# Kernel tuning notes

Hardware: AMD Instinct MI355X
Metric: run time of the kernel (lower is better)

The kernel has to match this reference:

```python
import jax, jax.numpy as jnp
import numpy as np

EMBED_DIM = 512
NUM_HEADS = 8
HEAD_DIM = EMBED_DIM // NUM_HEADS
SCALE = HEAD_DIM ** -0.5
B, N = 4, 2048


def setup_inputs() -> dict:
    key = jax.random.key(0)
    ks = jax.random.split(key, 6)
    x = jax.random.normal(ks[0], (B, N, EMBED_DIM), dtype=jnp.float32)
    mask = jnp.ones((B, N, N), dtype=jnp.int32)
    # nn.Linear params: weight [out, in], bias [out]
    lim_qkv = 1.0 / np.sqrt(EMBED_DIM)
    qkv_w = jax.random.uniform(ks[1], (3 * EMBED_DIM, EMBED_DIM), jnp.float32, -lim_qkv, lim_qkv)
    qkv_b = jax.random.uniform(ks[2], (3 * EMBED_DIM,), jnp.float32, -lim_qkv, lim_qkv)
    proj_w = jax.random.uniform(ks[3], (EMBED_DIM, EMBED_DIM), jnp.float32, -lim_qkv, lim_qkv)
    proj_b = jax.random.uniform(ks[4], (EMBED_DIM,), jnp.float32, -lim_qkv, lim_qkv)
    return {"x": x, "qkv_w": qkv_w, "qkv_b": qkv_b, "proj_w": proj_w, "proj_b": proj_b, "mask": mask}


def reference(x, qkv_w, qkv_b, proj_w, proj_b, mask):
    Bb, Nn, C = x.shape
    qkv = (jnp.einsum('bnc,oc->bno', x, qkv_w) + qkv_b).reshape(Bb, Nn, 3, NUM_HEADS, HEAD_DIM)
    qkv = jnp.transpose(qkv, (2, 0, 3, 1, 4))
    q, k, v = qkv[0], qkv[1], qkv[2]
    # full score matrix [B,H,N,N] (faithful to the unfused original)
    attn = jnp.einsum('bhnd,bhmd->bhnm', q, k) * SCALE
    attn = jnp.where(mask[:, None, :, :] == 0, -jnp.inf, attn)
    attn = jax.nn.softmax(attn, axis=-1)
    out = jnp.einsum('bhnm,bhmd->bhnd', attn, v)
    out = jnp.transpose(out, (0, 2, 1, 3)).reshape(Bb, Nn, C)
    out = jnp.einsum('bnc,oc->bno', out, proj_w) + proj_b
    return out
```

## Files before the change

kernel.cpp:

```cpp
#include <hip/hip_runtime.h>
#include <hip/hip_bf16.h>
#include <stdint.h>

#define NB 4
#define NH 8
#define SEQ 2048
#define HD 64
#define CDIM 512

using bf16 = __hip_bfloat16;
typedef __attribute__((ext_vector_type(8))) short short8;
typedef __attribute__((ext_vector_type(4))) short short4_t;
typedef __attribute__((ext_vector_type(4))) float f32x4;

#define NEG_BIG (-3.0e38f)
#define SOFT_C 0.18033688011112042f

__device__ __forceinline__ short bf16_bits(float x) {
  return __builtin_bit_cast(short, __float2bfloat16(x));
}

#define X4 1048576
#define Q4 196608
#define P4 65536
__global__ __launch_bounds__(256) void prep_cvt(const float* __restrict__ x,
                                                const float* __restrict__ wq,
                                                const float* __restrict__ wp,
                                                short* __restrict__ xb,
                                                short* __restrict__ wqb,
                                                short* __restrict__ wpb) {
  int idx = blockIdx.x * 256 + threadIdx.x;
  int stride = gridDim.x * 256;
  for (int i = idx; i < X4 + Q4 + P4; i += stride) {
    const float* src; short* dst; int off;
    if (i < X4)            { src = x;  dst = xb;  off = i; }
    else if (i < X4 + Q4)  { src = wq; dst = wqb; off = i - X4; }
    else                   { src = wp; dst = wpb; off = i - X4 - Q4; }
    f32x4 v = *(const f32x4*)(src + (size_t)off * 4);
    short4_t o;
    o[0] = bf16_bits(v[0]); o[1] = bf16_bits(v[1]);
    o[2] = bf16_bits(v[2]); o[3] = bf16_bits(v[3]);
    *(short4_t*)(dst + (size_t)off * 4) = o;
  }
}

__global__ __launch_bounds__(256) void qkv_union(const short* __restrict__ Xb,
                                                 const short* __restrict__ Wb,
                                                 const float* __restrict__ bias,
                                                 const int* __restrict__ mask,
                                                 unsigned long long* __restrict__ bits,
                                                 bf16* __restrict__ q,
                                                 bf16* __restrict__ k,
                                                 bf16* __restrict__ vt) {
  __shared__ short Alds[128][40];
  __shared__ short Blds[128][40];
  const int tid = threadIdx.x;
  const int lane = tid & 63;
  const int w = tid >> 6;

  if (blockIdx.x < 512) {
    int wave_g = blockIdx.x * 4 + w;
#pragma unroll 1
    for (int i = 0; i < 32; i++) {
      size_t c = (size_t)i * 2048 + wave_g;
      size_t base = c * 256;
      int v0 = mask[base + 0 * 64 + lane];
      int v1 = mask[base + 1 * 64 + lane];
      int v2 = mask[base + 2 * 64 + lane];
      int v3 = mask[base + 3 * 64 + lane];
      unsigned long long w0 = __ballot(v0 != 0);
      unsigned long long w1 = __ballot(v1 != 0);
      unsigned long long w2 = __ballot(v2 != 0);
      unsigned long long w3 = __ballot(v3 != 0);
      if (lane == 0) {
        bits[c * 4 + 0] = w0; bits[c * 4 + 1] = w1;
        bits[c * 4 + 2] = w2; bits[c * 4 + 3] = w3;
      }
    }
    return;
  }

  const int g = blockIdx.x - 512;
  const int wm = w >> 1, wn = w & 1;
  const int row0 = (g & 63) * 128;
  const int col0 = (g >> 6) * 128;

  f32x4 acc[4][4] = {};
  const int lr = tid >> 2;
  const int lc = (tid & 3) * 8;
  const int cl = lane & 15;
  const int koff = (lane >> 4) * 8;

  for (int kk = 0; kk < 512; kk += 32) {
    *(short8*)&Alds[lr][lc]      = *(const short8*)&Xb[(size_t)(row0 + lr) * 512 + kk + lc];
    *(short8*)&Alds[lr + 64][lc] = *(const short8*)&Xb[(size_t)(row0 + lr + 64) * 512 + kk + lc];
    *(short8*)&Blds[lr][lc]      = *(const short8*)&Wb[(size_t)(col0 + lr) * 512 + kk + lc];
    *(short8*)&Blds[lr + 64][lc] = *(const short8*)&Wb[(size_t)(col0 + lr + 64) * 512 + kk + lc];
    __syncthreads();
    short8 a[4], b[4];
#pragma unroll
    for (int i = 0; i < 4; i++) a[i] = *(const short8*)&Alds[wm * 64 + i * 16 + cl][koff];
#pragma unroll
    for (int j = 0; j < 4; j++) b[j] = *(const short8*)&Blds[wn * 64 + j * 16 + cl][koff];
#pragma unroll
    for (int i = 0; i < 4; i++)
#pragma unroll
      for (int j = 0; j < 4; j++)
        acc[i][j] = __builtin_amdgcn_mfma_f32_16x16x32_bf16(a[i], b[j], acc[i][j], 0, 0, 0);
    __syncthreads();
  }

#pragma unroll
  for (int i = 0; i < 4; i++) {
#pragma unroll
    for (int j = 0; j < 4; j++) {
      int col = col0 + wn * 64 + j * 16 + cl;
      float bv = bias[col];
      int which = col >> 9;
      int c = col & 511;
      int h = c >> 6, d = c & 63;
#pragma unroll
      for (int r = 0; r < 4; r++) {
        int row = row0 + wm * 64 + i * 16 + (lane >> 4) * 4 + r;
        int bb = row >> 11, n = row & 2047;
        float val = acc[i][j][r] + bv;
        size_t bh = (size_t)bb * NH + h;
        if (which == 0)      q[(bh * SEQ + n) * HD + d] = __float2bfloat16(val * SOFT_C);
        else if (which == 1) k[(bh * SEQ + n) * HD + d] = __float2bfloat16(val);
        else                 vt[(bh * HD + d) * SEQ + n] = __float2bfloat16(val);
      }
    }
  }
}

__global__ __launch_bounds__(256) void flash_attn(const bf16* __restrict__ qg,
                                                  const bf16* __restrict__ kg,
                                                  const bf16* __restrict__ vg,
                                                  const unsigned long long* __restrict__ mbits,
                                                  bf16* __restrict__ attn_out) {
  __shared__ short Klds[64][72];
  __shared__ short Vlds[64][72];
  __shared__ short Plds[4][16][72];
  __shared__ unsigned long long Mlds[64];

  const int tid = threadIdx.x;
  const int lane = tid & 63;
  const int w = tid >> 6;
  const int qt = blockIdx.x;
  const int h = blockIdx.y;
  const int b = blockIdx.z;

  const size_t bh = (size_t)b * NH + h;
  const bf16* qp = qg + bh * SEQ * HD;
  const bf16* kp = kg + bh * SEQ * HD;
  const bf16* vp = vg + bh * HD * SEQ;

  const int cl = lane & 15;
  const int quad = lane >> 4;
  const int koff = quad * 8;
  const int qrow_w = qt * 64 + w * 16;

  short8 aq0 = *(const short8*)&qp[(size_t)(qrow_w + cl) * HD + koff];
  short8 aq1 = *(const short8*)&qp[(size_t)(qrow_w + cl) * HD + 32 + koff];

  f32x4 o[4] = {};
  float l_l = 0.f;

  const int sr = tid >> 3;
  const int sc = (tid & 7) * 8;

  for (int kt = 0; kt < 32; kt++) {
    const int kb = kt * 64;
    *(short8*)&Klds[sr][sc]      = *(const short8*)&kp[(size_t)(kb + sr) * HD + sc];
    *(short8*)&Klds[sr + 32][sc] = *(const short8*)&kp[(size_t)(kb + sr + 32) * HD + sc];
    *(short8*)&Vlds[sr][sc]      = *(const short8*)&vp[(size_t)sr * SEQ + kb + sc];
    *(short8*)&Vlds[sr + 32][sc] = *(const short8*)&vp[(size_t)(sr + 32) * SEQ + kb + sc];
    if (tid < 64) Mlds[tid] = mbits[((size_t)b * SEQ + qt * 64 + tid) * (SEQ / 64) + kt];
    __syncthreads();

    f32x4 s[4];
#pragma unroll
    for (int nb = 0; nb < 4; nb++) {
      short8 k0 = *(const short8*)&Klds[nb * 16 + cl][koff];
      short8 k1 = *(const short8*)&Klds[nb * 16 + cl][32 + koff];
      f32x4 z = {0.f, 0.f, 0.f, 0.f};
      z = __builtin_amdgcn_mfma_f32_16x16x32_bf16(k0, aq0, z, 0, 0, 0);
      s[nb] = __builtin_amdgcn_mfma_f32_16x16x32_bf16(k1, aq1, z, 0, 0, 0);
    }

    unsigned long long wd = Mlds[w * 16 + cl];
    if (wd != ~0ULL) {
#pragma unroll
      for (int nb = 0; nb < 4; nb++)
#pragma unroll
        for (int r = 0; r < 4; r++)
          if (!((wd >> (nb * 16 + quad * 4 + r)) & 1ULL)) s[nb][r] = NEG_BIG;
    }

    float ps = 0.f;
#pragma unroll
    for (int nb = 0; nb < 4; nb++)
#pragma unroll
      for (int r = 0; r < 4; r++) {
        float p = exp2f(s[nb][r]);
        s[nb][r] = p;
        ps += p;
      }
    ps += __shfl_xor(ps, 16);
    ps += __shfl_xor(ps, 32);
    l_l += ps;

#pragma unroll
    for (int nb = 0; nb < 4; nb++) {
      short4_t pk;
      pk[0] = bf16_bits(s[nb][0]); pk[1] = bf16_bits(s[nb][1]);
      pk[2] = bf16_bits(s[nb][2]); pk[3] = bf16_bits(s[nb][3]);
      *(short4_t*)&Plds[w][cl][nb * 16 + quad * 4] = pk;
    }

#pragma unroll
    for (int ks = 0; ks < 2; ks++) {
      short8 pa = *(const short8*)&Plds[w][cl][ks * 32 + koff];
#pragma unroll
      for (int db = 0; db < 4; db++) {
        short8 vb = *(const short8*)&Vlds[db * 16 + cl][ks * 32 + koff];
        o[db] = __builtin_amdgcn_mfma_f32_16x16x32_bf16(pa, vb, o[db], 0, 0, 0);
      }
    }
    __syncthreads();
  }

  float inv = 1.0f / l_l;
#pragma unroll
  for (int r = 0; r < 4; r++) {
    float ir = __shfl(inv, (lane & 48) + quad * 4 + r);
    int row = qrow_w + quad * 4 + r;
#pragma unroll
    for (int db = 0; db < 4; db++) {
      float val = o[db][r] * ir;
      attn_out[((size_t)b * SEQ + row) * CDIM + h * 64 + db * 16 + cl] = __float2bfloat16(val);
    }
  }
}

__global__ __launch_bounds__(256) void proj_gemm(const bf16* __restrict__ X,
                                                 const short* __restrict__ Wb,
                                                 const float* __restrict__ bias,
                                                 float* __restrict__ out) {
  __shared__ short Alds[128][40];
  __shared__ short Blds[128][40];
  const int tid = threadIdx.x;
  const int lane = tid & 63;
  const int w = tid >> 6;
  const int wm = w >> 1, wn = w & 1;
  const int row0 = blockIdx.x * 128;
  const int col0 = blockIdx.y * 128;

  f32x4 acc[4][4] = {};
  const int lr = tid >> 2;
  const int lc = (tid & 3) * 8;
  const int cl = lane & 15;
  const int koff = (lane >> 4) * 8;

  for (int kk = 0; kk < 512; kk += 32) {
    *(short8*)&Alds[lr][lc]      = *(const short8*)&X[(size_t)(row0 + lr) * 512 + kk + lc];
    *(short8*)&Alds[lr + 64][lc] = *(const short8*)&X[(size_t)(row0 + lr + 64) * 512 + kk + lc];
    *(short8*)&Blds[lr][lc]      = *(const short8*)&Wb[(size_t)(col0 + lr) * 512 + kk + lc];
    *(short8*)&Blds[lr + 64][lc] = *(const short8*)&Wb[(size_t)(col0 + lr + 64) * 512 + kk + lc];
    __syncthreads();
    short8 a[4], b[4];
#pragma unroll
    for (int i = 0; i < 4; i++) a[i] = *(const short8*)&Alds[wm * 64 + i * 16 + cl][koff];
#pragma unroll
    for (int j = 0; j < 4; j++) b[j] = *(const short8*)&Blds[wn * 64 + j * 16 + cl][koff];
#pragma unroll
    for (int i = 0; i < 4; i++)
#pragma unroll
      for (int j = 0; j < 4; j++)
        acc[i][j] = __builtin_amdgcn_mfma_f32_16x16x32_bf16(a[i], b[j], acc[i][j], 0, 0, 0);
    __syncthreads();
  }

#pragma unroll
  for (int i = 0; i < 4; i++) {
#pragma unroll
    for (int j = 0; j < 4; j++) {
      int col = col0 + wn * 64 + j * 16 + cl;
      float bv = bias[col];
#pragma unroll
      for (int r = 0; r < 4; r++) {
        int row = row0 + wm * 64 + i * 16 + (lane >> 4) * 4 + r;
        out[(size_t)row * 512 + col] = acc[i][j][r] + bv;
      }
    }
  }
}

extern "C" void kernel_launch(void* const* d_in, const int* in_sizes, int n_in,
                              void* d_out, int out_size, void* d_ws, size_t ws_size,
                              hipStream_t stream) {
  const float* x      = (const float*)d_in[0];
  const float* qkv_w  = (const float*)d_in[1];
  const float* qkv_b  = (const float*)d_in[2];
  const float* proj_w = (const float*)d_in[3];
  const float* proj_b = (const float*)d_in[4];
  const int*   mask   = (const int*)d_in[5];
  float* out = (float*)d_out;

  char* ws = (char*)d_ws;
  bf16* q    = (bf16*)(ws);
  bf16* k    = (bf16*)(ws + 8388608);
  bf16* vt   = (bf16*)(ws + 16777216);
  bf16* attn = (bf16*)(ws + 25165824);
  short* xb  = (short*)(ws + 25165824);
  unsigned long long* mbits = (unsigned long long*)(ws + 33554432);
  short* wqb = (short*)(ws + 35651584);
  short* wpb = (short*)(ws + 37224448);

  prep_cvt<<<dim3(1280), 256, 0, stream>>>(x, qkv_w, proj_w, xb, wqb, wpb);
  qkv_union<<<dim3(512 + 768), 256, 0, stream>>>(xb, wqb, qkv_b, mask, mbits, q, k, vt);
  flash_attn<<<dim3(SEQ / 64, NH, NB), 256, 0, stream>>>(q, k, vt, mbits, attn);
  proj_gemm<<<dim3(64, 4), 256, 0, stream>>>(attn, wpb, proj_b, out);
}
```

Before: 257.7 us.

## Use direct global-to-LDS loads with XOR swizzle and transpose-friendly V store

The flash attention kernel now loads K and V tiles with global_load_lds straight into unpadded LDS and uses an XOR-swizzled column layout to avoid bank conflicts, replacing register-staged loads. The QKV projection swaps the MFMA operands for V tiles so each lane writes consecutive sequence positions into the transposed V buffer, aiming for better-coalesced stores. exp2f is replaced with the hardware exp2 intrinsic. The swizzle must line up between the direct-LDS store pattern and the reads, and the intrinsic skips the denormal and range handling that exp2f does.

```diff
diff --git a/kernel.cpp b/kernel.cpp
--- a/kernel.cpp
+++ b/kernel.cpp
@@ -18,6 +18,12 @@
 
 __device__ __forceinline__ short bf16_bits(float x) {
   return __builtin_bit_cast(short, __float2bfloat16(x));
+}
+
+__device__ __forceinline__ void gld_lds16(const void* g, void* l) {
+  __builtin_amdgcn_global_load_lds(
+      (const __attribute__((address_space(1))) unsigned int*)g,
+      (__attribute__((address_space(3))) unsigned int*)l, 16, 0, 0);
 }
 
 #define X4 1048576
@@ -84,12 +90,14 @@
   const int wm = w >> 1, wn = w & 1;
   const int row0 = (g & 63) * 128;
   const int col0 = (g >> 6) * 128;
+  const bool isv = (col0 >= 1024);
 
   f32x4 acc[4][4] = {};
   const int lr = tid >> 2;
   const int lc = (tid & 3) * 8;
   const int cl = lane & 15;
-  const int koff = (lane >> 4) * 8;
+  const int quad = lane >> 4;
+  const int koff = quad * 8;
 
   for (int kk = 0; kk < 512; kk += 32) {
     *(short8*)&Alds[lr][lc]      = *(const short8*)&Xb[(size_t)(row0 + lr) * 512 + kk + lc];
@@ -102,32 +110,60 @@
     for (int i = 0; i < 4; i++) a[i] = *(const short8*)&Alds[wm * 64 + i * 16 + cl][koff];
 #pragma unroll
     for (int j = 0; j < 4; j++) b[j] = *(const short8*)&Blds[wn * 64 + j * 16 + cl][koff];
-#pragma unroll
-    for (int i = 0; i < 4; i++)
-#pragma unroll
-      for (int j = 0; j < 4; j++)
-        acc[i][j] = __builtin_amdgcn_mfma_f32_16x16x32_bf16(a[i], b[j], acc[i][j], 0, 0, 0);
-    __syncthreads();
-  }
-
-#pragma unroll
-  for (int i = 0; i < 4; i++) {
-#pragma unroll
-    for (int j = 0; j < 4; j++) {
-      int col = col0 + wn * 64 + j * 16 + cl;
-      float bv = bias[col];
-      int which = col >> 9;
-      int c = col & 511;
-      int h = c >> 6, d = c & 63;
-#pragma unroll
-      for (int r = 0; r < 4; r++) {
-        int row = row0 + wm * 64 + i * 16 + (lane >> 4) * 4 + r;
-        int bb = row >> 11, n = row & 2047;
-        float val = acc[i][j][r] + bv;
-        size_t bh = (size_t)bb * NH + h;
-        if (which == 0)      q[(bh * SEQ + n) * HD + d] = __float2bfloat16(val * SOFT_C);
-        else if (which == 1) k[(bh * SEQ + n) * HD + d] = __float2bfloat16(val);
-        else                 vt[(bh * HD + d) * SEQ + n] = __float2bfloat16(val);
+    if (!isv) {
+#pragma unroll
+      for (int i = 0; i < 4; i++)
+#pragma unroll
+        for (int j = 0; j < 4; j++)
+          acc[i][j] = __builtin_amdgcn_mfma_f32_16x16x32_bf16(a[i], b[j], acc[i][j], 0, 0, 0);
+    } else {
+#pragma unroll
+      for (int i = 0; i < 4; i++)
+#pragma unroll
+        for (int j = 0; j < 4; j++)
+          acc[i][j] = __builtin_amdgcn_mfma_f32_16x16x32_bf16(b[j], a[i], acc[i][j], 0, 0, 0);
+    }
+    __syncthreads();
+  }
+
+  if (!isv) {
+#pragma unroll
+    for (int i = 0; i < 4; i++) {
+#pragma unroll
+      for (int j = 0; j < 4; j++) {
+        int col = col0 + wn * 64 + j * 16 + cl;
+        float bv = bias[col];
+        int which = col >> 9;
+        int c = col & 511;
+        int h = c >> 6, d = c & 63;
+#pragma unroll
+        for (int r = 0; r < 4; r++) {
+          int row = row0 + wm * 64 + i * 16 + quad * 4 + r;
+          int bb = row >> 11, n = row & 2047;
+          float val = acc[i][j][r] + bv;
+          size_t bh = (size_t)bb * NH + h;
+          if (which == 0)      q[(bh * SEQ + n) * HD + d] = __float2bfloat16(val * SOFT_C);
+          else                 k[(bh * SEQ + n) * HD + d] = __float2bfloat16(val);
+        }
+      }
+    }
+  } else {
+#pragma unroll
+    for (int i = 0; i < 4; i++) {
+#pragma unroll
+      for (int j = 0; j < 4; j++) {
+        int nrow = row0 + wm * 64 + i * 16 + cl;
+        int bb = nrow >> 11, n = nrow & 2047;
+#pragma unroll
+        for (int r = 0; r < 4; r++) {
+          int col = col0 + wn * 64 + j * 16 + quad * 4 + r;
+          float bv = bias[col];
+          int c = col & 511;
+          int h = c >> 6, d = c & 63;
+          float val = acc[i][j][r] + bv;
+          size_t bh = (size_t)bb * NH + h;
+          vt[(bh * HD + d) * SEQ + n] = __float2bfloat16(val);
+        }
       }
     }
   }
@@ -138,8 +174,8 @@
                                                   const bf16* __restrict__ vg,
                                                   const unsigned long long* __restrict__ mbits,
                                                   bf16* __restrict__ attn_out) {
-  __shared__ short Klds[64][72];
-  __shared__ short Vlds[64][72];
+  __shared__ short Klds[64][64];
+  __shared__ short Vlds[64][64];
   __shared__ short Plds[4][16][72];
   __shared__ unsigned long long Mlds[64];
 
@@ -160,29 +196,34 @@
   const int koff = quad * 8;
   const int qrow_w = qt * 64 + w * 16;
 
+  const int c0 = ((quad ^ (cl & 7)) * 8);
+
+  const int st_row = lane >> 3;
+  const int st_chunk = (lane & 7) ^ st_row;
+  const int st_col = st_chunk * 8;
+
   short8 aq0 = *(const short8*)&qp[(size_t)(qrow_w + cl) * HD + koff];
   short8 aq1 = *(const short8*)&qp[(size_t)(qrow_w + cl) * HD + 32 + koff];
 
   f32x4 o[4] = {};
   float l_l = 0.f;
 
-  const int sr = tid >> 3;
-  const int sc = (tid & 7) * 8;
-
   for (int kt = 0; kt < 32; kt++) {
     const int kb = kt * 64;
-    *(short8*)&Klds[sr][sc]      = *(const short8*)&kp[(size_t)(kb + sr) * HD + sc];
-    *(short8*)&Klds[sr + 32][sc] = *(const short8*)&kp[(size_t)(kb + sr + 32) * HD + sc];
-    *(short8*)&Vlds[sr][sc]      = *(const short8*)&vp[(size_t)sr * SEQ + kb + sc];
-    *(short8*)&Vlds[sr + 32][sc] = *(const short8*)&vp[(size_t)(sr + 32) * SEQ + kb + sc];
+#pragma unroll
+    for (int t = 0; t < 2; t++) {
+      int rbase = w * 16 + t * 8;
+      gld_lds16(&kp[(size_t)(kb + rbase + st_row) * HD + st_col], &Klds[rbase][0]);
+      gld_lds16(&vp[(size_t)(rbase + st_row) * SEQ + kb + st_col], &Vlds[rbase][0]);
+    }
     if (tid < 64) Mlds[tid] = mbits[((size_t)b * SEQ + qt * 64 + tid) * (SEQ / 64) + kt];
     __syncthreads();
 
     f32x4 s[4];
 #pragma unroll
     for (int nb = 0; nb < 4; nb++) {
-      short8 k0 = *(const short8*)&Klds[nb * 16 + cl][koff];
-      short8 k1 = *(const short8*)&Klds[nb * 16 + cl][32 + koff];
+      short8 k0 = *(const short8*)&Klds[nb * 16 + cl][c0];
+      short8 k1 = *(const short8*)&Klds[nb * 16 + cl][c0 ^ 32];
       f32x4 z = {0.f, 0.f, 0.f, 0.f};
       z = __builtin_amdgcn_mfma_f32_16x16x32_bf16(k0, aq0, z, 0, 0, 0);
       s[nb] = __builtin_amdgcn_mfma_f32_16x16x32_bf16(k1, aq1, z, 0, 0, 0);
@@ -202,7 +243,7 @@
     for (int nb = 0; nb < 4; nb++)
 #pragma unroll
       for (int r = 0; r < 4; r++) {
-        float p = exp2f(s[nb][r]);
+        float p = __builtin_amdgcn_exp2f(s[nb][r]);
         s[nb][r] = p;
         ps += p;
       }
@@ -221,9 +262,10 @@
 #pragma unroll
     for (int ks = 0; ks < 2; ks++) {
       short8 pa = *(const short8*)&Plds[w][cl][ks * 32 + koff];
+      const int vc = c0 ^ (ks * 32);
 #pragma unroll
       for (int db = 0; db < 4; db++) {
-        short8 vb = *(const short8*)&Vlds[db * 16 + cl][ks * 32 + koff];
+        short8 vb = *(const short8*)&Vlds[db * 16 + cl][vc];
         o[db] = __builtin_amdgcn_mfma_f32_16x16x32_bf16(pa, vb, o[db], 0, 0, 0);
       }
     }
```

Result: faster. 229.3 us (-11.0%).
